# Kernel tuning notes

Measured on AMD Instinct MI355X. Metric: run time of the kernel, lower is better.

## Reference

```python
import jax, jax.numpy as jnp
import numpy as np

# static config (matches init_kwargs)
H, W = 56, 56
T = 4            # temporal_dims
C = 256          # dim1
NH = 8           # num_heads
WS = 7           # window_size
SS = 3           # shift_size
HID = 1024       # mlp hidden = 4*C
N = WS * WS      # tokens per window
EPS = 1e-5


def _ln(x, g, b):
    m = jnp.mean(x, axis=-1, keepdims=True)
    v = jnp.mean((x - m) ** 2, axis=-1, keepdims=True)
    return (x - m) * jax.lax.rsqrt(v + EPS) * g + b


def _window_partition(x, ws):
    B, Hh, Ww, Cc = x.shape
    x = x.reshape(B, Hh // ws, ws, Ww // ws, ws, Cc)
    return x.transpose(0, 1, 3, 2, 4, 5).reshape(-1, ws, ws, Cc)


def _window_reverse(win, ws, Hh, Ww):
    B = win.shape[0] // ((Hh // ws) * (Ww // ws))
    x = win.reshape(B, Hh // ws, Ww // ws, ws, ws, -1)
    return x.transpose(0, 1, 3, 2, 4, 5).reshape(B, Hh, Ww, -1)


def _rel_pos_index(ws):
    coords = np.stack(np.meshgrid(np.arange(ws), np.arange(ws), indexing='ij'))
    cf = coords.reshape(2, -1)
    rel = (cf[:, :, None] - cf[:, None, :]).transpose(1, 2, 0).astype(np.int64)
    rel[..., 0] += ws - 1
    rel[..., 1] += ws - 1
    rel[..., 0] *= 2 * ws - 1
    return rel.sum(-1)  # (ws*ws, ws*ws)


def _shift_mask():
    # identical to the torch buffer built in __init__ (on temporal_dims*H x W grid)
    img = np.zeros((T * H, W), dtype=np.float32)
    cnt = 0
    for hs in (slice(0, -WS), slice(-WS, -SS), slice(-SS, None)):
        for wsl in (slice(0, -WS), slice(-WS, -SS), slice(-SS, None)):
            img[hs, wsl] = cnt
            cnt += 1
    mw = img.reshape((T * H) // WS, WS, W // WS, WS).transpose(0, 2, 1, 3).reshape(-1, N)
    am = mw[:, None, :] - mw[:, :, None]
    return np.where(am != 0, np.float32(-100.0), np.float32(0.0))  # (nW, N, N)

_RPI = _rel_pos_index(WS)
_ATTN_MASK = _shift_mask()


def setup_inputs() -> dict:
    key = jax.random.key(0)
    ks = jax.random.split(key, 8)
    B = 4
    s = 0.02
    return {
        'x1': jax.random.normal(ks[0], (B, T * H * W, C), jnp.float32),
        'x2': jax.random.normal(ks[1], (B, H * W, C), jnp.float32),
        'norm1_g': jnp.ones((C,), jnp.float32),
        'norm1_b': jnp.zeros((C,), jnp.float32),
        'qkv_w': jax.random.normal(ks[2], (3 * C, C), jnp.float32) * s,
        'qkv_b': jnp.zeros((3 * C,), jnp.float32),
        'proj_w': jax.random.normal(ks[3], (C, C), jnp.float32) * s,
        'proj_b': jnp.zeros((C,), jnp.float32),
        'rpb_table': jax.random.normal(ks[4], ((2 * WS - 1) ** 2, NH), jnp.float32) * s,
        'norm2_g': jnp.ones((C,), jnp.float32),
        'norm2_b': jnp.zeros((C,), jnp.float32),
        'fc1_w': jax.random.normal(ks[5], (HID, C), jnp.float32) * s,
        'fc1_b': jnp.zeros((HID,), jnp.float32),
        'fc2_w': jax.random.normal(ks[6], (C, HID), jnp.float32) * s,
        'fc2_b': jnp.zeros((C,), jnp.float32),
    }


def _block(x1, norm1_g, norm1_b, qkv_w, qkv_b, proj_w, proj_b, rpb_table,
           norm2_g, norm2_b, fc1_w, fc1_b, fc2_w, fc2_b):
    B, L, _ = x1.shape
    hd = C // NH
    shortcut = x1
    x = _ln(x1, norm1_g, norm1_b).reshape(B, T * H, W, C)
    # cyclic shift + window partition
    x = jnp.roll(x, shift=(-SS, -SS), axis=(1, 2))
    xw = _window_partition(x, WS).reshape(-1, N, C)          # (B*nW, N, C)
    Bw = xw.shape[0]
    nW = Bw // B
    # window attention with relative position bias + shift mask
    qkv = (xw @ qkv_w.T + qkv_b).reshape(Bw, N, 3, NH, hd).transpose(2, 0, 3, 1, 4)
    q, k, v = qkv[0], qkv[1], qkv[2]
    attn = jnp.einsum('bhnd,bhmd->bhnm', q * (hd ** -0.5), k)
    bias = rpb_table[jnp.asarray(_RPI)].transpose(2, 0, 1)    # (NH, N, N)
    attn = attn + bias[None]
    mask = jnp.asarray(_ATTN_MASK)
    attn = attn.reshape(B, nW, NH, N, N) + mask[None, :, None]
    attn = jax.nn.softmax(attn.reshape(Bw, NH, N, N), axis=-1)
    y = jnp.einsum('bhnm,bhmd->bhnd', attn, v).transpose(0, 2, 1, 3).reshape(Bw, N, C)
    y = y @ proj_w.T + proj_b
    # reverse windows + un-shift
    y = _window_reverse(y.reshape(-1, WS, WS, C), WS, T * H, W)
    y = jnp.roll(y, shift=(SS, SS), axis=(1, 2)).reshape(B, L, C)
    out = y
    x1 = shortcut + y
    # MLP (GELU exact, as torch nn.GELU default)
    h = _ln(x1, norm2_g, norm2_b)
    h = jax.nn.gelu(h @ fc1_w.T + fc1_b, approximate=False)
    x1 = x1 + (h @ fc2_w.T + fc2_b)
    return x1, out


def reference(x1, x2, norm1_g, norm1_b, qkv_w, qkv_b, proj_w, proj_b, rpb_table,
              norm2_g, norm2_b, fc1_w, fc1_b, fc2_w, fc2_b):
    # last_view=True: x2 is reshaped but unused by the executed path
    return _block(x1, norm1_g, norm1_b, qkv_w, qkv_b, proj_w, proj_b, rpb_table,
                  norm2_g, norm2_b, fc1_w, fc1_b, fc2_w, fc2_b)
```

## Files before the change

kernel.cpp:

```cpp
#include <hip/hip_runtime.h>
#include <hip/hip_bf16.h>
#include <cmath>

#define CDIM 256
#define TPW 49
#define NWIN 1024
#define MTOK (NWIN * TPW)
#define NHEAD 8
#define GH 224
#define GW 56
#define PLD 72

typedef __attribute__((ext_vector_type(8))) __bf16 bf16x8;
typedef __attribute__((ext_vector_type(4))) float f32x4;

__device__ __forceinline__ __bf16 to_bf16(float f) {
    __hip_bfloat16 h = __float2bfloat16(f);
    return *(__bf16*)&h;
}

__device__ __forceinline__ void async_copy16(const void* g, void* l) {
    __builtin_amdgcn_global_load_lds(
        (const __attribute__((address_space(1))) void*)g,
        (__attribute__((address_space(3))) void*)l, 16, 0, 0);
}

__device__ __forceinline__ float wave_sum(float v) {
    v += __shfl_down(v, 32);
    v += __shfl_down(v, 16);
    v += __shfl_down(v, 8);
    v += __shfl_down(v, 4);
    v += __shfl_down(v, 2);
    v += __shfl_down(v, 1);
    return v;
}

__global__ __launch_bounds__(256) void castall_kernel(
    const float* __restrict__ qw, const float* __restrict__ pw,
    const float* __restrict__ f1, const float* __restrict__ f2,
    __hip_bfloat16* __restrict__ dst)
{
    const int i = blockIdx.x * 256 + threadIdx.x;
    float v;
    if (i < 196608) v = qw[i];
    else if (i < 262144) v = pw[i - 196608];
    else if (i < 524288) v = f1[i - 262144];
    else v = f2[i - 524288];
    dst[i] = __float2bfloat16(v);
}

__global__ __launch_bounds__(256) void cb_kernel(
    const float* __restrict__ rpb, float* __restrict__ cbt)
{
    const int cls = blockIdx.x >> 3, head = blockIdx.x & 7;
    for (int e = threadIdx.x; e < 64 * 64; e += 256) {
        const int m = e >> 6, n = e & 63;
        float v;
        if (m >= 49 || n >= 49) v = -30000.0f;
        else {
            const int in_ = n / 7, jn = n - in_ * 7;
            const int im = m / 7, jm = m - im * 7;
            v = rpb[((in_ - im + 6) * 13 + (jn - jm + 6)) * 8 + head];
            const int hn = (cls & 2) ? 217 + in_ : in_;
            const int wn = (cls & 1) ? 49 + jn : jn;
            const int hm = (cls & 2) ? 217 + im : im;
            const int wm = (cls & 1) ? 49 + jm : jm;
            const int rn = (hn < 217 ? 0 : (hn < 221 ? 3 : 6)) + (wn < 49 ? 0 : (wn < 53 ? 1 : 2));
            const int rm = (hm < 217 ? 0 : (hm < 221 ? 3 : 6)) + (wm < 49 ? 0 : (wm < 53 ? 1 : 2));
            if (rn != rm) v -= 100.0f;
        }
        cbt[((long)blockIdx.x * 64 + m) * 64 + n] = v;
    }
}

__global__ __launch_bounds__(256) void ln1_window_kernel(
    const float* __restrict__ x1, const float* __restrict__ g,
    const float* __restrict__ b, __hip_bfloat16* __restrict__ out)
{
    const int wave = threadIdx.x >> 6, lane = threadIdx.x & 63;
    const int t = blockIdx.x * 4 + wave;
    const int bw = t / TPW, n = t - bw * TPW;
    const int bb = bw >> 8, wi = bw & 255;
    const int hb = wi >> 3, wb = wi & 7;
    const int i = n / 7, j = n - i * 7;
    int h0 = hb * 7 + i + 3; if (h0 >= GH) h0 -= GH;
    int w0 = wb * 7 + j + 3; if (w0 >= GW) w0 -= GW;
    const long src = ((long)(bb * GH + h0) * GW + w0) * CDIM + lane * 4;
    const float4 v = *(const float4*)(x1 + src);
    float s = v.x + v.y + v.z + v.w;
    s = wave_sum(s);
    const float mean = __shfl(s, 0) * (1.0f / 256.0f);
    const float4 d = { v.x - mean, v.y - mean, v.z - mean, v.w - mean };
    float s2 = d.x * d.x + d.y * d.y + d.z * d.z + d.w * d.w;
    s2 = wave_sum(s2);
    const float rstd = rsqrtf(__shfl(s2, 0) * (1.0f / 256.0f) + 1e-5f);
    const float4 g4 = *(const float4*)(g + lane * 4);
    const float4 b4 = *(const float4*)(b + lane * 4);
    short4 pk;
    { __bf16 h = to_bf16(d.x * rstd * g4.x + b4.x); pk.x = *(short*)&h; }
    { __bf16 h = to_bf16(d.y * rstd * g4.y + b4.y); pk.y = *(short*)&h; }
    { __bf16 h = to_bf16(d.z * rstd * g4.z + b4.z); pk.z = *(short*)&h; }
    { __bf16 h = to_bf16(d.w * rstd * g4.w + b4.w); pk.w = *(short*)&h; }
    *(short4*)((short*)out + (long)t * CDIM + lane * 4) = pk;
}

__global__ __launch_bounds__(256) void ln_kernel(
    const float* __restrict__ x, const float* __restrict__ g,
    const float* __restrict__ b, __hip_bfloat16* __restrict__ out)
{
    const int wave = threadIdx.x >> 6, lane = threadIdx.x & 63;
    const long t = (long)blockIdx.x * 4 + wave;
    const float4 v = *(const float4*)(x + t * CDIM + lane * 4);
    float s = v.x + v.y + v.z + v.w;
    s = wave_sum(s);
    const float mean = __shfl(s, 0) * (1.0f / 256.0f);
    const float4 d = { v.x - mean, v.y - mean, v.z - mean, v.w - mean };
    float s2 = d.x * d.x + d.y * d.y + d.z * d.z + d.w * d.w;
    s2 = wave_sum(s2);
    const float rstd = rsqrtf(__shfl(s2, 0) * (1.0f / 256.0f) + 1e-5f);
    const float4 g4 = *(const float4*)(g + lane * 4);
    const float4 b4 = *(const float4*)(b + lane * 4);
    short4 pk;
    { __bf16 h = to_bf16(d.x * rstd * g4.x + b4.x); pk.x = *(short*)&h; }
    { __bf16 h = to_bf16(d.y * rstd * g4.y + b4.y); pk.y = *(short*)&h; }
    { __bf16 h = to_bf16(d.z * rstd * g4.z + b4.z); pk.z = *(short*)&h; }
    { __bf16 h = to_bf16(d.w * rstd * g4.w + b4.w); pk.w = *(short*)&h; }
    *(short4*)((short*)out + t * CDIM + lane * 4) = pk;
}

template <int EPI, typename OutT>
__global__ __launch_bounds__(256) void gemm_mfma(
    const __hip_bfloat16* __restrict__ X, const __hip_bfloat16* __restrict__ W,
    const float* __restrict__ bias, OutT* __restrict__ Y,
    int M, int K, int N, const float* __restrict__ res, float* __restrict__ Y2)
{
    __shared__ __hip_bfloat16 As[2][128 * 32];
    __shared__ __hip_bfloat16 Bs[2][128 * 32];
    const int tid = threadIdx.x;
    const int wave = tid >> 6, lane = tid & 63;
    const int nwg = gridDim.x * gridDim.y;
    const int L = blockIdx.y * gridDim.x + blockIdx.x;
    const int cpx = nwg >> 3;
    const int orig = (L & 7) * cpx + (L >> 3);
    const int bxx = orig % gridDim.x;
    const int byy = orig / gridDim.x;
    const int bm = byy * 128, bn = bxx * 128;
    const int wm = (wave & 1) * 64, wn = (wave >> 1) * 64;
    const int m16 = lane & 15, quad = lane >> 4;
    const int srow = lane >> 2;
    const int scol = (lane & 3) * 8;

    const __hip_bfloat16* xb = X + (long)bm * K + scol;
    const __hip_bfloat16* wb = W + (long)bn * K + scol;
    const int rg0 = wave * 2, rg1 = wave * 2 + 1;
    const long xr0 = (long)(rg0 * 16 + srow) * K, xr1 = (long)(rg1 * 16 + srow) * K;

    f32x4 acc[4][4] = {};

    async_copy16(xb + xr0, (char*)As[0] + rg0 * 1024);
    async_copy16(wb + xr0, (char*)Bs[0] + rg0 * 1024);
    async_copy16(xb + xr1, (char*)As[0] + rg1 * 1024);
    async_copy16(wb + xr1, (char*)Bs[0] + rg1 * 1024);
    __syncthreads();

    int cur = 0;
    for (int k0 = 0; k0 < K; k0 += 32) {
        if (k0 + 32 < K) {
            const int nxt = cur ^ 1;
            async_copy16(xb + xr0 + k0 + 32, (char*)As[nxt] + rg0 * 1024);
            async_copy16(wb + xr0 + k0 + 32, (char*)Bs[nxt] + rg0 * 1024);
            async_copy16(xb + xr1 + k0 + 32, (char*)As[nxt] + rg1 * 1024);
            async_copy16(wb + xr1 + k0 + 32, (char*)Bs[nxt] + rg1 * 1024);
        }
        bf16x8 af[4], bf[4];
#pragma unroll
        for (int i = 0; i < 4; ++i)
            af[i] = *(const bf16x8*)&As[cur][(wm + i * 16 + m16) * 32 + quad * 8];
#pragma unroll
        for (int j = 0; j < 4; ++j)
            bf[j] = *(const bf16x8*)&Bs[cur][(wn + j * 16 + m16) * 32 + quad * 8];
#pragma unroll
        for (int i = 0; i < 4; ++i)
#pragma unroll
            for (int j = 0; j < 4; ++j)
                acc[i][j] = __builtin_amdgcn_mfma_f32_16x16x32_bf16(bf[j], af[i], acc[i][j], 0, 0, 0);
        __syncthreads();
        cur ^= 1;
    }

#pragma unroll
    for (int i = 0; i < 4; ++i) {
        const long row = bm + wm + i * 16 + m16;
        long drow = row;
        if (EPI == 3) {
            const unsigned t = (unsigned)row;
            const unsigned bw_ = t / 49u;
            const unsigned n_ = t - bw_ * 49u;
            const unsigned bb = bw_ >> 8, wi = bw_ & 255u;
            const unsigned hb = wi >> 3, wbl = wi & 7u;
            const unsigned ii = n_ / 7u, jj = n_ - ii * 7u;
            int h0 = hb * 7 + ii + 3; if (h0 >= GH) h0 -= GH;
            int w0 = wbl * 7 + jj + 3; if (w0 >= GW) w0 -= GW;
            drow = (long)bb * (GH * GW) + h0 * GW + w0;
        }
#pragma unroll
        for (int j = 0; j < 4; ++j) {
            const int col = bn + wn + j * 16 + quad * 4;
            const float4 b4 = *(const float4*)&bias[col];
            float v[4];
            v[0] = acc[i][j][0] + b4.x;
            v[1] = acc[i][j][1] + b4.y;
            v[2] = acc[i][j][2] + b4.z;
            v[3] = acc[i][j][3] + b4.w;
            if (EPI == 1) {
#pragma unroll
                for (int r = 0; r < 4; ++r)
                    v[r] = 0.5f * v[r] * (1.0f + erff(v[r] * 0.70710678118654752f));
            }
            if (EPI == 0 || EPI == 1) {
                short4 pk;
                { __bf16 h = to_bf16(v[0]); pk.x = *(short*)&h; }
                { __bf16 h = to_bf16(v[1]); pk.y = *(short*)&h; }
                { __bf16 h = to_bf16(v[2]); pk.z = *(short*)&h; }
                { __bf16 h = to_bf16(v[3]); pk.w = *(short*)&h; }
                *(short4*)((short*)Y + row * N + col) = pk;
            } else if (EPI == 2) {
                const float4 r4 = *(const float4*)(res + row * N + col);
                float4 o4 = { v[0] + r4.x, v[1] + r4.y, v[2] + r4.z, v[3] + r4.w };
                *(float4*)((float*)Y + row * N + col) = o4;
            } else if (EPI == 3) {
                const long a = drow * 256 + col;
                const float4 x4 = *(const float4*)(res + a);
                float4 y4 = { v[0], v[1], v[2], v[3] };
                *(float4*)(Y2 + a) = y4;
                float4 s4 = { v[0] + x4.x, v[1] + x4.y, v[2] + x4.z, v[3] + x4.w };
                *(float4*)((float*)Y + a) = s4;
            }
        }
    }
}

__global__ __launch_bounds__(256) void attn_mfma_kernel(
    const __hip_bfloat16* __restrict__ qkv,
    const float* __restrict__ cbt,
    __hip_bfloat16* __restrict__ yout)
{
    __shared__ __bf16 P[4][64][PLD];
    const int tid = threadIdx.x;
    const int wave = tid >> 6, lane = tid & 63;
    const int bw = blockIdx.x >> 1;
    const int head = (blockIdx.x & 1) * 4 + wave;
    const int m16 = lane & 15, quad = lane >> 4;
    const int wi = bw & 255;
    const int hb = wi >> 3, wb = wi & 7;
    const int cls = ((hb == 31) ? 2 : 0) + ((wb == 7) ? 1 : 0);

    const __bf16* qb = (const __bf16*)qkv + (long)bw * TPW * 768 + head * 32;

    bf16x8 qf[4], kf[4];
#pragma unroll
    for (int i = 0; i < 4; ++i) {
        const int n = i * 16 + m16;
        bf16x8 q = {}, k = {};
        if (n < TPW) {
            const __bf16* p = qb + (long)n * 768 + quad * 8;
            q = *(const bf16x8*)p;
            k = *(const bf16x8*)(p + 256);
        }
        qf[i] = q; kf[i] = k;
    }

    bf16x8 vf[2][2];
#pragma unroll
    for (int jt = 0; jt < 2; ++jt)
#pragma unroll
        for (int kt = 0; kt < 2; ++kt) {
            bf16x8 v = {};
#pragma unroll
            for (int j = 0; j < 8; ++j) {
                const int tok = kt * 32 + quad * 8 + j;
                if (tok < TPW) v[j] = qb[(long)tok * 768 + 512 + jt * 16 + m16];
            }
            vf[jt][kt] = v;
        }

    f32x4 s[4][4] = {};
#pragma unroll
    for (int i = 0; i < 4; ++i)
#pragma unroll
        for (int j = 0; j < 4; ++j)
            s[i][j] = __builtin_amdgcn_mfma_f32_16x16x32_bf16(qf[i], kf[j], s[i][j], 0, 0, 0);

    const float* cb = cbt + (long)(cls * 8 + head) * 64 * 64;
#pragma unroll
    for (int j = 0; j < 4; ++j) {
        const int m = j * 16 + m16;
#pragma unroll
        for (int i = 0; i < 4; ++i) {
            const float4 c = *(const float4*)(cb + m * 64 + i * 16 + quad * 4);
            s[i][j][0] = s[i][j][0] * 0.17677669529663687f + c.x;
            s[i][j][1] = s[i][j][1] * 0.17677669529663687f + c.y;
            s[i][j][2] = s[i][j][2] * 0.17677669529663687f + c.z;
            s[i][j][3] = s[i][j][3] * 0.17677669529663687f + c.w;
        }
    }

#pragma unroll
    for (int i = 0; i < 4; ++i) {
#pragma unroll
        for (int r = 0; r < 4; ++r) {
            float mx = fmaxf(fmaxf(s[i][0][r], s[i][1][r]), fmaxf(s[i][2][r], s[i][3][r]));
            mx = fmaxf(mx, __shfl_xor(mx, 1));
            mx = fmaxf(mx, __shfl_xor(mx, 2));
            mx = fmaxf(mx, __shfl_xor(mx, 4));
            mx = fmaxf(mx, __shfl_xor(mx, 8));
            float sum = 0.0f;
#pragma unroll
            for (int j = 0; j < 4; ++j) {
                const float e = __expf(s[i][j][r] - mx);
                s[i][j][r] = e;
                sum += e;
            }
            sum += __shfl_xor(sum, 1);
            sum += __shfl_xor(sum, 2);
            sum += __shfl_xor(sum, 4);
            sum += __shfl_xor(sum, 8);
            const float inv = 1.0f / sum;
#pragma unroll
            for (int j = 0; j < 4; ++j)
                P[wave][i * 16 + quad * 4 + r][j * 16 + m16] = to_bf16(s[i][j][r] * inv);
        }
    }

    f32x4 o[4][2] = {};
#pragma unroll
    for (int kt = 0; kt < 2; ++kt)
#pragma unroll
        for (int i = 0; i < 4; ++i) {
            const bf16x8 pf = *(const bf16x8*)&P[wave][i * 16 + m16][kt * 32 + quad * 8];
#pragma unroll
            for (int jt = 0; jt < 2; ++jt)
                o[i][jt] = __builtin_amdgcn_mfma_f32_16x16x32_bf16(vf[jt][kt], pf, o[i][jt], 0, 0, 0);
        }

#pragma unroll
    for (int i = 0; i < 4; ++i) {
        const int tok = i * 16 + m16;
        if (tok < TPW) {
#pragma unroll
            for (int jt = 0; jt < 2; ++jt) {
                short4 pk;
                { __bf16 h = to_bf16(o[i][jt][0]); pk.x = *(short*)&h; }
                { __bf16 h = to_bf16(o[i][jt][1]); pk.y = *(short*)&h; }
                { __bf16 h = to_bf16(o[i][jt][2]); pk.z = *(short*)&h; }
                { __bf16 h = to_bf16(o[i][jt][3]); pk.w = *(short*)&h; }
                *(short4*)((short*)yout + ((long)bw * TPW + tok) * CDIM + head * 32 + jt * 16 + quad * 4) = pk;
            }
        }
    }
}

extern "C" void kernel_launch(void* const* d_in, const int* in_sizes, int n_in,
                              void* d_out, int out_size, void* d_ws, size_t ws_size,
                              hipStream_t stream) {
    (void)in_sizes; (void)n_in; (void)out_size; (void)ws_size;
    const float* x1     = (const float*)d_in[0];
    const float* n1g    = (const float*)d_in[2];
    const float* n1b    = (const float*)d_in[3];
    const float* qkv_w  = (const float*)d_in[4];
    const float* qkv_b  = (const float*)d_in[5];
    const float* proj_w = (const float*)d_in[6];
    const float* proj_b = (const float*)d_in[7];
    const float* rpb    = (const float*)d_in[8];
    const float* n2g    = (const float*)d_in[9];
    const float* n2b    = (const float*)d_in[10];
    const float* fc1_w  = (const float*)d_in[11];
    const float* fc1_b  = (const float*)d_in[12];
    const float* fc2_w  = (const float*)d_in[13];
    const float* fc2_b  = (const float*)d_in[14];

    float* out_x1 = (float*)d_out;
    float* out_y  = out_x1 + (long)MTOK * CDIM;

    char* ws = (char*)d_ws;
    const size_t SZ_A   = (size_t)MTOK * CDIM * sizeof(__hip_bfloat16);
    const size_t SZ_BIG = (size_t)MTOK * 1024 * sizeof(__hip_bfloat16);
    __hip_bfloat16* A    = (__hip_bfloat16*)ws;
    char*           BIG  = ws + SZ_A;
    __hip_bfloat16* qkvb = (__hip_bfloat16*)BIG;
    __hip_bfloat16* H1   = (__hip_bfloat16*)BIG;
    __hip_bfloat16* wB   = (__hip_bfloat16*)(ws + SZ_A + SZ_BIG);
    __hip_bfloat16* qkv_wb  = wB;
    __hip_bfloat16* proj_wb = wB + 196608;
    __hip_bfloat16* fc1_wb  = wB + 262144;
    __hip_bfloat16* fc2_wb  = wB + 524288;
    float* cbt = (float*)(wB + 786432);

    castall_kernel<<<3072, 256, 0, stream>>>(qkv_w, proj_w, fc1_w, fc2_w, wB);
    cb_kernel<<<32, 256, 0, stream>>>(rpb, cbt);
    ln1_window_kernel<<<MTOK / 4, 256, 0, stream>>>(x1, n1g, n1b, A);
    gemm_mfma<0, __hip_bfloat16><<<dim3(768 / 128, MTOK / 128), 256, 0, stream>>>(
        A, qkv_wb, qkv_b, qkvb, MTOK, CDIM, 768, nullptr, nullptr);
    attn_mfma_kernel<<<NWIN * 2, 256, 0, stream>>>(qkvb, cbt, A);
    gemm_mfma<3, float><<<dim3(256 / 128, MTOK / 128), 256, 0, stream>>>(
        A, proj_wb, proj_b, out_x1, MTOK, CDIM, CDIM, x1, out_y);
    ln_kernel<<<MTOK / 4, 256, 0, stream>>>(out_x1, n2g, n2b, A);
    gemm_mfma<1, __hip_bfloat16><<<dim3(1024 / 128, MTOK / 128), 256, 0, stream>>>(
        A, fc1_wb, fc1_b, H1, MTOK, CDIM, 1024, nullptr, nullptr);
    gemm_mfma<2, float><<<dim3(256 / 128, MTOK / 128), 256, 0, stream>>>(
        H1, fc2_wb, fc2_b, out_x1, MTOK, 1024, CDIM, out_x1, nullptr);
}
```

Baseline: 463.0 us.

## Triple-buffer GEMM LDS tiles with explicit vmcnt waits for deeper prefetch

The MFMA GEMM moves from a double-buffered to a triple-buffered LDS pipeline. Loads run two K-steps ahead, and partial s_waitcnt vmcnt counts replace full __syncthreads so global-to-LDS copies overlap compute longer. This raises LDS use per block, which may lower occupancy. It also depends on hand-counted vmcnt values matching the number of outstanding async loads per thread.

```diff
diff --git a/kernel.cpp b/kernel.cpp
--- a/kernel.cpp
+++ b/kernel.cpp
@@ -134,8 +134,8 @@
     const float* __restrict__ bias, OutT* __restrict__ Y,
     int M, int K, int N, const float* __restrict__ res, float* __restrict__ Y2)
 {
-    __shared__ __hip_bfloat16 As[2][128 * 32];
-    __shared__ __hip_bfloat16 Bs[2][128 * 32];
+    __shared__ __hip_bfloat16 As[3][128 * 32];
+    __shared__ __hip_bfloat16 Bs[3][128 * 32];
     const int tid = threadIdx.x;
     const int wave = tid >> 6, lane = tid & 63;
     const int nwg = gridDim.x * gridDim.y;
@@ -156,36 +156,54 @@
     const long xr0 = (long)(rg0 * 16 + srow) * K, xr1 = (long)(rg1 * 16 + srow) * K;
 
     f32x4 acc[4][4] = {};
+    const int NK = K >> 5;
 
     async_copy16(xb + xr0, (char*)As[0] + rg0 * 1024);
     async_copy16(wb + xr0, (char*)Bs[0] + rg0 * 1024);
     async_copy16(xb + xr1, (char*)As[0] + rg1 * 1024);
     async_copy16(wb + xr1, (char*)Bs[0] + rg1 * 1024);
-    __syncthreads();
-
-    int cur = 0;
-    for (int k0 = 0; k0 < K; k0 += 32) {
-        if (k0 + 32 < K) {
-            const int nxt = cur ^ 1;
-            async_copy16(xb + xr0 + k0 + 32, (char*)As[nxt] + rg0 * 1024);
-            async_copy16(wb + xr0 + k0 + 32, (char*)Bs[nxt] + rg0 * 1024);
-            async_copy16(xb + xr1 + k0 + 32, (char*)As[nxt] + rg1 * 1024);
-            async_copy16(wb + xr1 + k0 + 32, (char*)Bs[nxt] + rg1 * 1024);
-        }
+    async_copy16(xb + xr0 + 32, (char*)As[1] + rg0 * 1024);
+    async_copy16(wb + xr0 + 32, (char*)Bs[1] + rg0 * 1024);
+    async_copy16(xb + xr1 + 32, (char*)As[1] + rg1 * 1024);
+    async_copy16(wb + xr1 + 32, (char*)Bs[1] + rg1 * 1024);
+    asm volatile("s_waitcnt vmcnt(4)" ::: "memory");
+    __builtin_amdgcn_sched_barrier(0);
+    __builtin_amdgcn_s_barrier();
+
+    for (int k = 0; k < NK; ++k) {
+        const int kb = k % 3;
+        if (k + 2 < NK) {
+            const int nb = (k + 2) % 3;
+            const long ko = (long)(k + 2) * 32;
+            async_copy16(xb + xr0 + ko, (char*)As[nb] + rg0 * 1024);
+            async_copy16(wb + xr0 + ko, (char*)Bs[nb] + rg0 * 1024);
+            async_copy16(xb + xr1 + ko, (char*)As[nb] + rg1 * 1024);
+            async_copy16(wb + xr1 + ko, (char*)Bs[nb] + rg1 * 1024);
+            asm volatile("s_waitcnt vmcnt(8)" ::: "memory");
+        } else if (k + 1 < NK) {
+            asm volatile("s_waitcnt vmcnt(4)" ::: "memory");
+        } else {
+            asm volatile("s_waitcnt vmcnt(0)" ::: "memory");
+        }
+        __builtin_amdgcn_sched_barrier(0);
+        __builtin_amdgcn_s_barrier();
+
         bf16x8 af[4], bf[4];
 #pragma unroll
         for (int i = 0; i < 4; ++i)
-            af[i] = *(const bf16x8*)&As[cur][(wm + i * 16 + m16) * 32 + quad * 8];
+            af[i] = *(const bf16x8*)&As[kb][(wm + i * 16 + m16) * 32 + quad * 8];
 #pragma unroll
         for (int j = 0; j < 4; ++j)
-            bf[j] = *(const bf16x8*)&Bs[cur][(wn + j * 16 + m16) * 32 + quad * 8];
+            bf[j] = *(const bf16x8*)&Bs[kb][(wn + j * 16 + m16) * 32 + quad * 8];
 #pragma unroll
         for (int i = 0; i < 4; ++i)
 #pragma unroll
             for (int j = 0; j < 4; ++j)
                 acc[i][j] = __builtin_amdgcn_mfma_f32_16x16x32_bf16(bf[j], af[i], acc[i][j], 0, 0, 0);
-        __syncthreads();
-        cur ^= 1;
+
+        asm volatile("s_waitcnt lgkmcnt(0)" ::: "memory");
+        __builtin_amdgcn_sched_barrier(0);
+        __builtin_amdgcn_s_barrier();
     }
 
 #pragma unroll
```

Measured after the change: 459.6 us. No clear change (-0.7%).

## Widen GEMM tiles to 128x256 with 512-thread blocks

Applied to the files above, without the earlier changes.

The MFMA GEMM now uses eight waves per block and a 128x256 output tile, so each block loads the A tile once and reuses it across twice as many output columns. The shared-memory B buffer doubles, the load mapping is rewritten so each thread issues one A and two B async copies, and the launch grids are halved in N. This trades fewer blocks (lower occupancy and fewer workgroups for the 256-wide GEMMs) for less redundant loading of the A operand.

```diff
diff --git a/kernel.cpp b/kernel.cpp
--- a/kernel.cpp
+++ b/kernel.cpp
@@ -129,13 +129,13 @@
 }
 
 template <int EPI, typename OutT>
-__global__ __launch_bounds__(256) void gemm_mfma(
+__global__ __launch_bounds__(512) void gemm_mfma(
     const __hip_bfloat16* __restrict__ X, const __hip_bfloat16* __restrict__ W,
     const float* __restrict__ bias, OutT* __restrict__ Y,
     int M, int K, int N, const float* __restrict__ res, float* __restrict__ Y2)
 {
     __shared__ __hip_bfloat16 As[2][128 * 32];
-    __shared__ __hip_bfloat16 Bs[2][128 * 32];
+    __shared__ __hip_bfloat16 Bs[2][256 * 32];
     const int tid = threadIdx.x;
     const int wave = tid >> 6, lane = tid & 63;
     const int nwg = gridDim.x * gridDim.y;
@@ -144,33 +144,31 @@
     const int orig = (L & 7) * cpx + (L >> 3);
     const int bxx = orig % gridDim.x;
     const int byy = orig / gridDim.x;
-    const int bm = byy * 128, bn = bxx * 128;
+    const int bm = byy * 128, bn = bxx * 256;
     const int wm = (wave & 1) * 64, wn = (wave >> 1) * 64;
     const int m16 = lane & 15, quad = lane >> 4;
-    const int srow = lane >> 2;
-    const int scol = (lane & 3) * 8;
-
-    const __hip_bfloat16* xb = X + (long)bm * K + scol;
-    const __hip_bfloat16* wb = W + (long)bn * K + scol;
-    const int rg0 = wave * 2, rg1 = wave * 2 + 1;
-    const long xr0 = (long)(rg0 * 16 + srow) * K, xr1 = (long)(rg1 * 16 + srow) * K;
+    const int srow = tid >> 2;
+    const int scol = (tid & 3) * 8;
+
+    const __hip_bfloat16* xrow  = X + (long)(bm + srow) * K + scol;
+    const __hip_bfloat16* wrow0 = W + (long)(bn + srow) * K + scol;
+    const __hip_bfloat16* wrow1 = W + (long)(bn + 128 + srow) * K + scol;
+    const int wb1k = wave * 1024;
 
     f32x4 acc[4][4] = {};
 
-    async_copy16(xb + xr0, (char*)As[0] + rg0 * 1024);
-    async_copy16(wb + xr0, (char*)Bs[0] + rg0 * 1024);
-    async_copy16(xb + xr1, (char*)As[0] + rg1 * 1024);
-    async_copy16(wb + xr1, (char*)Bs[0] + rg1 * 1024);
+    async_copy16(xrow,  (char*)As[0] + wb1k);
+    async_copy16(wrow0, (char*)Bs[0] + wb1k);
+    async_copy16(wrow1, (char*)Bs[0] + 8192 + wb1k);
     __syncthreads();
 
     int cur = 0;
     for (int k0 = 0; k0 < K; k0 += 32) {
         if (k0 + 32 < K) {
             const int nxt = cur ^ 1;
-            async_copy16(xb + xr0 + k0 + 32, (char*)As[nxt] + rg0 * 1024);
-            async_copy16(wb + xr0 + k0 + 32, (char*)Bs[nxt] + rg0 * 1024);
-            async_copy16(xb + xr1 + k0 + 32, (char*)As[nxt] + rg1 * 1024);
-            async_copy16(wb + xr1 + k0 + 32, (char*)Bs[nxt] + rg1 * 1024);
+            async_copy16(xrow + k0 + 32,  (char*)As[nxt] + wb1k);
+            async_copy16(wrow0 + k0 + 32, (char*)Bs[nxt] + wb1k);
+            async_copy16(wrow1 + k0 + 32, (char*)Bs[nxt] + 8192 + wb1k);
         }
         bf16x8 af[4], bf[4];
 #pragma unroll
@@ -399,14 +397,14 @@
     castall_kernel<<<3072, 256, 0, stream>>>(qkv_w, proj_w, fc1_w, fc2_w, wB);
     cb_kernel<<<32, 256, 0, stream>>>(rpb, cbt);
     ln1_window_kernel<<<MTOK / 4, 256, 0, stream>>>(x1, n1g, n1b, A);
-    gemm_mfma<0, __hip_bfloat16><<<dim3(768 / 128, MTOK / 128), 256, 0, stream>>>(
+    gemm_mfma<0, __hip_bfloat16><<<dim3(768 / 256, MTOK / 128), 512, 0, stream>>>(
         A, qkv_wb, qkv_b, qkvb, MTOK, CDIM, 768, nullptr, nullptr);
     attn_mfma_kernel<<<NWIN * 2, 256, 0, stream>>>(qkvb, cbt, A);
-    gemm_mfma<3, float><<<dim3(256 / 128, MTOK / 128), 256, 0, stream>>>(
+    gemm_mfma<3, float><<<dim3(1, MTOK / 128), 512, 0, stream>>>(
         A, proj_wb, proj_b, out_x1, MTOK, CDIM, CDIM, x1, out_y);
     ln_kernel<<<MTOK / 4, 256, 0, stream>>>(out_x1, n2g, n2b, A);
-    gemm_mfma<1, __hip_bfloat16><<<dim3(1024 / 128, MTOK / 128), 256, 0, stream>>>(
+    gemm_mfma<1, __hip_bfloat16><<<dim3(1024 / 256, MTOK / 128), 512, 0, stream>>>(
         A, fc1_wb, fc1_b, H1, MTOK, CDIM, 1024, nullptr, nullptr);
-    gemm_mfma<2, float><<<dim3(256 / 128, MTOK / 128), 256, 0, stream>>>(
+    gemm_mfma<2, float><<<dim3(1, MTOK / 128), 512, 0, stream>>>(
         H1, fc2_wb, fc2_b, out_x1, MTOK, 1024, CDIM, out_x1, nullptr);
 }
```

Result: faster. 438.1 us (-5.4%).
